# Kernel optimization log

Measured on AMD Instinct MI355X. Metric: run time of the kernel, lower is better.

The kernel has to match this reference:

```python
import jax, jax.numpy as jnp
import numpy as np

V = 50000
K = 24
NB = 10
P = (K - 1) * 9  # 207 pose-blend coefficients
# canonical SMPL kinematic tree (parent[0] is unused / root)
SMPL_PARENT = np.array([0, 0, 0, 0, 1, 2, 3, 4, 5, 6, 7, 8, 9, 9, 9, 12, 13, 14, 16, 17, 18, 19, 20, 21], dtype=np.int64)


def setup_inputs() -> dict:
    key = jax.random.key(0)
    ks = jax.random.split(key, 8)
    betas = jax.random.normal(ks[0], (NB,), dtype=jnp.float32)
    pose = jax.random.normal(ks[1], (K, 3), dtype=jnp.float32) * 0.3
    trans = jax.random.normal(ks[2], (3,), dtype=jnp.float32)
    shapedirs = jax.random.normal(ks[3], (V, 3, NB), dtype=jnp.float32) * 0.01
    v_template = jax.random.normal(ks[4], (V, 3), dtype=jnp.float32)
    J_regressor = jax.random.uniform(ks[5], (K, V), dtype=jnp.float32)
    J_regressor = J_regressor / jnp.sum(J_regressor, axis=1, keepdims=True)
    weights = jax.random.uniform(ks[6], (V, K), dtype=jnp.float32)
    weights = weights / jnp.sum(weights, axis=1, keepdims=True)
    posedirs = jax.random.normal(ks[7], (V, 3, P), dtype=jnp.float32) * 0.01
    return {"betas": betas, "pose": pose, "trans": trans, "shapedirs": shapedirs,
            "v_template": v_template, "J_regressor": J_regressor, "weights": weights,
            "posedirs": posedirs, "parent": SMPL_PARENT}


def rodrigues(r):
    """Axis-angle [K,3] -> rotation matrices [K,3,3]."""
    theta = jnp.linalg.norm(r + 1e-8, axis=-1, keepdims=True)  # [K,1]
    r_hat = r / theta
    x, y, z = r_hat[:, 0], r_hat[:, 1], r_hat[:, 2]
    zero = jnp.zeros_like(x)
    m = jnp.stack([zero, -z, y, z, zero, -x, -y, x, zero], axis=1).reshape(-1, 3, 3)
    cos = jnp.cos(theta)[:, :, None]
    sin = jnp.sin(theta)[:, :, None]
    eye = jnp.eye(3, dtype=r.dtype)[None]
    outer = r_hat[:, :, None] * r_hat[:, None, :]
    return cos * eye + (1.0 - cos) * outer + sin * m


def smpl_forward(betas, pose, trans, shapedirs, v_template, J_regressor, weights, posedirs, parent):
    parent = np.asarray(parent)
    nJ = parent.shape[0]
    v_shaped = jnp.einsum('vki,i->vk', shapedirs, betas) + v_template  # [V,3]
    J = J_regressor @ v_shaped                                          # [K,3]
    R = rodrigues(pose.reshape(-1, 3))                                  # [K,3,3]
    lrotmin = (R[1:] - jnp.eye(3, dtype=R.dtype)[None]).reshape(-1)     # [207]
    v_posed = v_shaped + jnp.einsum('vkp,p->vk', posedirs, lrotmin)

    bottom = jnp.array([[0.0, 0.0, 0.0, 1.0]], dtype=R.dtype)
    def make_A(Ri, t):  # [3,3],[3] -> [4,4]
        return jnp.concatenate([jnp.concatenate([Ri, t[:, None]], axis=1), bottom], axis=0)

    G = [make_A(R[0], J[0])]
    for i in range(1, nJ):  # fixed 24-joint tree, small static loop
        p = int(parent[i])
        G.append(G[p] @ make_A(R[i], J[i] - J[p]))
    stacked = jnp.stack(G, axis=0)                                      # [K,4,4]

    Jh = jnp.concatenate([J, jnp.zeros((nJ, 1), dtype=J.dtype)], axis=1)[:, :, None]  # [K,4,1]
    corr = stacked @ Jh                                                 # [K,4,1]
    pack = jnp.concatenate([jnp.zeros((nJ, 4, 3), dtype=J.dtype), corr], axis=2)
    results = stacked - pack                                            # [K,4,4]

    T = jnp.einsum('vj,jab->vab', weights, results)                     # [V,4,4]
    rest = jnp.concatenate([v_posed, jnp.ones((v_posed.shape[0], 1), dtype=v_posed.dtype)], axis=1)
    v = jnp.einsum('vab,vb->va', T, rest)[:, :3]
    return v + trans[None, :]


def reference(betas, pose, trans, shapedirs, v_template, J_regressor, weights, posedirs, parent):
    return smpl_forward(betas, pose, trans, shapedirs, v_template, J_regressor, weights, posedirs, parent)
```

## Files before the change

### kernel.cpp

```cpp
#include <hip/hip_runtime.h>

#define NV 50000
#define NJ 24
#define NBETA 10
#define NP 207
#define NROWS 150000

#define K1_BLOCKS 196

#define VPB 32
#define RPB 96
#define GPB 24
#define K3_BLOCKS 1563

#define PARTIAL_OFF 0
#define LROT_OFF    14336
#define M_OFF       14592

__device__ const int d_par[NJ] = {0,0,0,0,1,2,3,4,5,6,7,8,9,9,9,12,13,14,16,17,18,19,20,21};
__device__ const int d_lvl[NJ] = {0,1,1,1,2,2,2,3,3,3,4,4,4,4,4,5,5,5,6,6,7,7,8,8};

__global__ __launch_bounds__(256) void k1_partialJ(
    const float* __restrict__ betas, const float* __restrict__ shapedirs,
    const float* __restrict__ v_template, const float* __restrict__ Jreg,
    float* __restrict__ ws)
{
    __shared__ float sd[256 * 30];
    __shared__ float vt[256 * 3];
    __shared__ float bet[NBETA];
    __shared__ float red[4 * 72];

    const int t = threadIdx.x;
    const int blk = blockIdx.x;
    if (t < NBETA) bet[t] = betas[t];

    const int vbase = blk * 256;
    const int nv    = min(256, NV - vbase);
    {
        const int nf4 = (nv * 30) >> 2;
        const float4* sdg = (const float4*)(shapedirs + (size_t)vbase * 30);
        for (int i = t; i < nf4; i += 256) ((float4*)sd)[i] = sdg[i];
        const float* vtg = v_template + (size_t)vbase * 3;
        const int nf3 = nv * 3;
        for (int i = t; i < nf3; i += 256) vt[i] = vtg[i];
    }
    __syncthreads();

    float accJ[72];
#pragma unroll
    for (int q = 0; q < 72; q++) accJ[q] = 0.f;

    const int v = vbase + t;
    if (v < NV) {
        float vs0 = vt[t * 3 + 0], vs1 = vt[t * 3 + 1], vs2 = vt[t * 3 + 2];
#pragma unroll
        for (int i = 0; i < NBETA; i++) {
            const float b = bet[i];
            vs0 += sd[t * 30 + 0 * 10 + i] * b;
            vs1 += sd[t * 30 + 1 * 10 + i] * b;
            vs2 += sd[t * 30 + 2 * 10 + i] * b;
        }
#pragma unroll
        for (int j = 0; j < NJ; j++) {
            const float w = Jreg[(size_t)j * NV + v];
            accJ[j * 3 + 0] += w * vs0;
            accJ[j * 3 + 1] += w * vs1;
            accJ[j * 3 + 2] += w * vs2;
        }
    }

    const int lane = t & 63, wv = t >> 6;
#pragma unroll
    for (int q = 0; q < 72; q++) {
        float x = accJ[q];
#pragma unroll
        for (int m = 1; m < 64; m <<= 1) x += __shfl_xor(x, m);
        if (lane == 0) red[wv * 72 + q] = x;
    }
    __syncthreads();
    if (t < 72)
        ws[PARTIAL_OFF + blk * 72 + t] = red[t] + red[72 + t] + red[144 + t] + red[216 + t];
}

__global__ __launch_bounds__(256) void k2_small(
    const float* __restrict__ pose, float* __restrict__ ws)
{
    __shared__ float Jl[NJ * 3];
    __shared__ float Rl[NJ * 9];
    __shared__ float Gl[NJ * 12];
    const int t = threadIdx.x;

    if (t < 72) {
        float s0 = 0.f, s1 = 0.f;
        for (int b = 0; b < K1_BLOCKS; b += 2) {
            s0 += ws[PARTIAL_OFF + b * 72 + t];
            s1 += ws[PARTIAL_OFF + (b + 1) * 72 + t];
        }
        Jl[t] = s0 + s1;
    }
    __syncthreads();

    if (t < NJ) {
        const float x = pose[t * 3 + 0], y = pose[t * 3 + 1], z = pose[t * 3 + 2];
        const float ex = x + 1e-8f, ey = y + 1e-8f, ez = z + 1e-8f;
        const float theta = sqrtf(ex * ex + ey * ey + ez * ez);
        const float inv = 1.f / theta;
        const float rx = x * inv, ry = y * inv, rz = z * inv;
        const float c = cosf(theta), s = sinf(theta), omc = 1.f - c;
        float R[9];
        R[0] = c + omc * rx * rx;      R[1] = omc * rx * ry - s * rz; R[2] = omc * rx * rz + s * ry;
        R[3] = omc * ry * rx + s * rz; R[4] = c + omc * ry * ry;      R[5] = omc * ry * rz - s * rx;
        R[6] = omc * rz * rx - s * ry; R[7] = omc * rz * ry + s * rx; R[8] = c + omc * rz * rz;
#pragma unroll
        for (int q = 0; q < 9; q++) Rl[t * 9 + q] = R[q];
        if (t >= 1) {
#pragma unroll
            for (int q = 0; q < 9; q++)
                ws[LROT_OFF + (t - 1) * 9 + q] = R[q] - ((q == 0 || q == 4 || q == 8) ? 1.f : 0.f);
        }
    }
    __syncthreads();

    for (int L = 0; L < 9; L++) {
        if (t < NJ && d_lvl[t] == L) {
            if (t == 0) {
#pragma unroll
                for (int r = 0; r < 3; r++) {
                    Gl[r * 4 + 0] = Rl[r * 3 + 0];
                    Gl[r * 4 + 1] = Rl[r * 3 + 1];
                    Gl[r * 4 + 2] = Rl[r * 3 + 2];
                    Gl[r * 4 + 3] = Jl[r];
                }
            } else {
                const int p = d_par[t];
                const float tx = Jl[t * 3 + 0] - Jl[p * 3 + 0];
                const float ty = Jl[t * 3 + 1] - Jl[p * 3 + 1];
                const float tz = Jl[t * 3 + 2] - Jl[p * 3 + 2];
#pragma unroll
                for (int r = 0; r < 3; r++) {
                    const float g0 = Gl[p * 12 + r * 4 + 0];
                    const float g1 = Gl[p * 12 + r * 4 + 1];
                    const float g2 = Gl[p * 12 + r * 4 + 2];
                    const float g3 = Gl[p * 12 + r * 4 + 3];
                    Gl[t * 12 + r * 4 + 0] = g0 * Rl[t * 9 + 0] + g1 * Rl[t * 9 + 3] + g2 * Rl[t * 9 + 6];
                    Gl[t * 12 + r * 4 + 1] = g0 * Rl[t * 9 + 1] + g1 * Rl[t * 9 + 4] + g2 * Rl[t * 9 + 7];
                    Gl[t * 12 + r * 4 + 2] = g0 * Rl[t * 9 + 2] + g1 * Rl[t * 9 + 5] + g2 * Rl[t * 9 + 8];
                    Gl[t * 12 + r * 4 + 3] = g0 * tx + g1 * ty + g2 * tz + g3;
                }
            }
        }
        __syncthreads();
    }

    if (t < NJ) {
        const float jx = Jl[t * 3 + 0], jy = Jl[t * 3 + 1], jz = Jl[t * 3 + 2];
#pragma unroll
        for (int r = 0; r < 3; r++) {
            const float g0 = Gl[t * 12 + r * 4 + 0];
            const float g1 = Gl[t * 12 + r * 4 + 1];
            const float g2 = Gl[t * 12 + r * 4 + 2];
            const float g3 = Gl[t * 12 + r * 4 + 3];
            ws[M_OFF + t * 12 + r * 4 + 0] = g0;
            ws[M_OFF + t * 12 + r * 4 + 1] = g1;
            ws[M_OFF + t * 12 + r * 4 + 2] = g2;
            ws[M_OFF + t * 12 + r * 4 + 3] = g3 - (g0 * jx + g1 * jy + g2 * jz);
        }
    }
}

__global__ __launch_bounds__(256) void k3_fused(
    const float* __restrict__ betas, const float* __restrict__ trans,
    const float* __restrict__ shapedirs, const float* __restrict__ v_template,
    const float* __restrict__ weights, const float* __restrict__ posedirs,
    const float* __restrict__ ws, float* __restrict__ out)
{
    __shared__ float vposed[RPB];
    __shared__ float Ml[288];

    const int t = threadIdx.x;
    const int lane = t & 63, wv = t >> 6;
    const int l16 = lane & 15, g = lane >> 4;
    const int blk = blockIdx.x;

    Ml[t] = ws[M_OFF + t];
    if (t < 32) Ml[256 + t] = ws[M_OFF + 256 + t];

    float lrk[12];
#pragma unroll
    for (int k = 0; k < 12; k++) lrk[k] = ws[LROT_OFF + k * 16 + l16];
    const float lr12 = (l16 < 15) ? ws[LROT_OFF + 192 + l16] : 0.f;
    const float bet  = (l16 < NBETA) ? betas[l16] : 0.f;

    const int gbase = blk * GPB + wv * 6;
#pragma unroll
    for (int i = 0; i < 6; i += 2) {
        const int rowA = (gbase + i) * 4 + g;
        const int rowB = rowA + 4;
        const bool okA = rowA < NROWS;
        const bool okB = rowB < NROWS;

        float va[12], vb[12];
        float tA = 0.f, tB = 0.f, sA = 0.f, sB = 0.f;
        if (okA) {
            const float* pa = posedirs + (size_t)rowA * NP;
#pragma unroll
            for (int k = 0; k < 12; k++) va[k] = pa[k * 16 + l16];
            if (l16 < 15)    tA = pa[192 + l16];
            if (l16 < NBETA) sA = shapedirs[(size_t)rowA * NBETA + l16];
        } else {
#pragma unroll
            for (int k = 0; k < 12; k++) va[k] = 0.f;
        }
        if (okB) {
            const float* pb = posedirs + (size_t)rowB * NP;
#pragma unroll
            for (int k = 0; k < 12; k++) vb[k] = pb[k * 16 + l16];
            if (l16 < 15)    tB = pb[192 + l16];
            if (l16 < NBETA) sB = shapedirs[(size_t)rowB * NBETA + l16];
        } else {
#pragma unroll
            for (int k = 0; k < 12; k++) vb[k] = 0.f;
        }

        float accA = tA * lr12 + sA * bet;
        float accB = tB * lr12 + sB * bet;
#pragma unroll
        for (int k = 0; k < 12; k++) accA += va[k] * lrk[k];
#pragma unroll
        for (int k = 0; k < 12; k++) accB += vb[k] * lrk[k];
#pragma unroll
        for (int m = 1; m < 16; m <<= 1) {
            accA += __shfl_xor(accA, m);
            accB += __shfl_xor(accB, m);
        }
        if (l16 == 0) {
            if (okA) vposed[rowA - blk * RPB] = accA + v_template[rowA];
            if (okB) vposed[rowB - blk * RPB] = accB + v_template[rowB];
        }
    }
    __syncthreads();

    if (t < VPB) {
        const int v = blk * VPB + t;
        if (v < NV) {
            const float4* w4 = (const float4*)(weights + (size_t)v * 24);
            float wj[24];
#pragma unroll
            for (int q = 0; q < 6; q++) {
                const float4 w = w4[q];
                wj[q * 4 + 0] = w.x; wj[q * 4 + 1] = w.y;
                wj[q * 4 + 2] = w.z; wj[q * 4 + 3] = w.w;
            }
            float T[12];
#pragma unroll
            for (int q = 0; q < 12; q++) T[q] = 0.f;
#pragma unroll
            for (int j = 0; j < NJ; j++) {
                const float w = wj[j];
#pragma unroll
                for (int q = 0; q < 12; q++) T[q] += w * Ml[j * 12 + q];
            }
            const float p0 = vposed[t * 3 + 0];
            const float p1 = vposed[t * 3 + 1];
            const float p2 = vposed[t * 3 + 2];
            out[(size_t)v * 3 + 0] = T[0] * p0 + T[1] * p1 + T[2]  * p2 + T[3]  + trans[0];
            out[(size_t)v * 3 + 1] = T[4] * p0 + T[5] * p1 + T[6]  * p2 + T[7]  + trans[1];
            out[(size_t)v * 3 + 2] = T[8] * p0 + T[9] * p1 + T[10] * p2 + T[11] + trans[2];
        }
    }
}

extern "C" void kernel_launch(void* const* d_in, const int* in_sizes, int n_in,
                              void* d_out, int out_size, void* d_ws, size_t ws_size,
                              hipStream_t stream) {
    const float* betas      = (const float*)d_in[0];
    const float* pose       = (const float*)d_in[1];
    const float* trans      = (const float*)d_in[2];
    const float* shapedirs  = (const float*)d_in[3];
    const float* v_template = (const float*)d_in[4];
    const float* Jreg       = (const float*)d_in[5];
    const float* weights    = (const float*)d_in[6];
    const float* posedirs   = (const float*)d_in[7];
    float* ws  = (float*)d_ws;
    float* out = (float*)d_out;

    k1_partialJ<<<dim3(K1_BLOCKS), dim3(256), 0, stream>>>(betas, shapedirs, v_template, Jreg, ws);
    k2_small<<<dim3(1), dim3(256), 0, stream>>>(pose, ws);
    k3_fused<<<dim3(K3_BLOCKS), dim3(256), 0, stream>>>(
        betas, trans, shapedirs, v_template, weights, posedirs, ws, out);
}
```

Before: 55.69 us.

## Load posedirs as float4 per row-group of four rows with whole-wave reduction

The pose-blend GEMV now treats four consecutive posedirs rows (828 floats) as one contiguous block that a whole 64-lane wave reads with float4 loads. The lrot coefficients are replicated four times in the workspace so each lane's float4 lines up with them, and lane-range predicates route each partial product to one of four row accumulators. The goal is fewer, wider, fully coalesced memory transactions on the dominant posedirs stream. In exchange it adds a full 64-lane butterfly reduction over eight accumulators, predicated adds, and moves the v_template add into the skinning stage.

```diff
diff --git a/kernel.cpp b/kernel.cpp
--- a/kernel.cpp
+++ b/kernel.cpp
@@ -5,6 +5,7 @@
 #define NBETA 10
 #define NP 207
 #define NROWS 150000
+#define ROWGROUPS 37500
 
 #define K1_BLOCKS 196
 
@@ -14,8 +15,8 @@
 #define K3_BLOCKS 1563
 
 #define PARTIAL_OFF 0
-#define LROT_OFF    14336
-#define M_OFF       14592
+#define LROT4_OFF   14592
+#define M_OFF       15424
 
 __device__ const int d_par[NJ] = {0,0,0,0,1,2,3,4,5,6,7,8,9,9,9,12,13,14,16,17,18,19,20,21};
 __device__ const int d_lvl[NJ] = {0,1,1,1,2,2,2,3,3,3,4,4,4,4,4,5,5,5,6,6,7,7,8,8};
@@ -88,6 +89,7 @@
     __shared__ float Jl[NJ * 3];
     __shared__ float Rl[NJ * 9];
     __shared__ float Gl[NJ * 12];
+    __shared__ float lrotl[NP];
     const int t = threadIdx.x;
 
     if (t < 72) {
@@ -116,10 +118,18 @@
         if (t >= 1) {
 #pragma unroll
             for (int q = 0; q < 9; q++)
-                ws[LROT_OFF + (t - 1) * 9 + q] = R[q] - ((q == 0 || q == 4 || q == 8) ? 1.f : 0.f);
-        }
-    }
-    __syncthreads();
+                lrotl[(t - 1) * 9 + q] = R[q] - ((q == 0 || q == 4 || q == 8) ? 1.f : 0.f);
+        }
+    }
+    __syncthreads();
+
+    for (int i = t; i < 4 * NP; i += 256) {
+        int c = i;
+        if (c >= 3 * NP) c -= 3 * NP;
+        else if (c >= 2 * NP) c -= 2 * NP;
+        else if (c >= NP) c -= NP;
+        ws[LROT4_OFF + i] = lrotl[c];
+    }
 
     for (int L = 0; L < 9; L++) {
         if (t < NJ && d_lvl[t] == L) {
@@ -179,63 +189,96 @@
 
     const int t = threadIdx.x;
     const int lane = t & 63, wv = t >> 6;
-    const int l16 = lane & 15, g = lane >> 4;
     const int blk = blockIdx.x;
 
     Ml[t] = ws[M_OFF + t];
     if (t < 32) Ml[256 + t] = ws[M_OFF + 256 + t];
 
-    float lrk[12];
-#pragma unroll
-    for (int k = 0; k < 12; k++) lrk[k] = ws[LROT_OFF + k * 16 + l16];
-    const float lr12 = (l16 < 15) ? ws[LROT_OFF + 192 + l16] : 0.f;
-    const float bet  = (l16 < NBETA) ? betas[l16] : 0.f;
+    const float4 z4 = {0.f, 0.f, 0.f, 0.f};
+
+    const float4* E4 = (const float4*)(ws + LROT4_OFF);
+    const float4 e40 = E4[lane];
+    const float4 e41 = E4[64 + lane];
+    const float4 e42 = E4[128 + lane];
+    const float4 e43 = (lane < 15) ? E4[192 + lane] : z4;
+
+    const int bcol = (lane < 10) ? lane : (lane < 20) ? lane - 10 : (lane < 30) ? lane - 20 : lane - 30;
+    const float bscal = (lane < 40) ? betas[bcol] : 0.f;
+
+    auto accum = [&](const float4& q0, const float4& q1, const float4& q2, const float4& q3,
+                     float sv, float& a0, float& a1, float& a2, float& a3) {
+        {
+            const float v0 = q0.x * e40.x, v1 = q0.y * e40.y, v2 = q0.z * e40.z, v3 = q0.w * e40.w;
+            const float s = v0 + v1 + v2;
+            if (lane < 52) a0 += s; else a1 += s;
+            if (lane < 51) a0 += v3; else a1 += v3;
+        }
+        {
+            const float v0 = q1.x * e41.x, v1 = q1.y * e41.y, v2 = q1.z * e41.z, v3 = q1.w * e41.w;
+            const float s01 = v0 + v1, s23 = v2 + v3;
+            if (lane < 40) a1 += s01; else a2 += s01;
+            if (lane < 39) a1 += s23; else a2 += s23;
+        }
+        {
+            const float v0 = q2.x * e42.x, v1 = q2.y * e42.y, v2 = q2.z * e42.z, v3 = q2.w * e42.w;
+            const float s123 = v1 + v2 + v3;
+            if (lane < 28) a2 += v0; else a3 += v0;
+            if (lane < 27) a2 += s123; else a3 += s123;
+        }
+        if (lane < 15) a3 += q3.x * e43.x + q3.y * e43.y + q3.z * e43.z + q3.w * e43.w;
+        {
+            const float v = sv * bscal;
+            if (lane < 10) a0 += v;
+            else if (lane < 20) a1 += v;
+            else if (lane < 30) a2 += v;
+            else if (lane < 40) a3 += v;
+        }
+    };
 
     const int gbase = blk * GPB + wv * 6;
 #pragma unroll
     for (int i = 0; i < 6; i += 2) {
-        const int rowA = (gbase + i) * 4 + g;
-        const int rowB = rowA + 4;
-        const bool okA = rowA < NROWS;
-        const bool okB = rowB < NROWS;
-
-        float va[12], vb[12];
-        float tA = 0.f, tB = 0.f, sA = 0.f, sB = 0.f;
+        const int gA = gbase + i, gB = gA + 1;
+        const bool okA = gA < ROWGROUPS, okB = gB < ROWGROUPS;
+
+        float4 pa0, pa1, pa2, pa3, pb0, pb1, pb2, pb3;
+        float sa = 0.f, sb = 0.f;
         if (okA) {
-            const float* pa = posedirs + (size_t)rowA * NP;
-#pragma unroll
-            for (int k = 0; k < 12; k++) va[k] = pa[k * 16 + l16];
-            if (l16 < 15)    tA = pa[192 + l16];
-            if (l16 < NBETA) sA = shapedirs[(size_t)rowA * NBETA + l16];
-        } else {
-#pragma unroll
-            for (int k = 0; k < 12; k++) va[k] = 0.f;
-        }
+            const float4* G = (const float4*)posedirs + (size_t)gA * 207;
+            pa0 = G[lane]; pa1 = G[64 + lane]; pa2 = G[128 + lane];
+            pa3 = (lane < 15) ? G[192 + lane] : z4;
+            sa  = (lane < 40) ? shapedirs[(size_t)gA * 40 + lane] : 0.f;
+        } else { pa0 = pa1 = pa2 = pa3 = z4; }
         if (okB) {
-            const float* pb = posedirs + (size_t)rowB * NP;
-#pragma unroll
-            for (int k = 0; k < 12; k++) vb[k] = pb[k * 16 + l16];
-            if (l16 < 15)    tB = pb[192 + l16];
-            if (l16 < NBETA) sB = shapedirs[(size_t)rowB * NBETA + l16];
-        } else {
-#pragma unroll
-            for (int k = 0; k < 12; k++) vb[k] = 0.f;
-        }
-
-        float accA = tA * lr12 + sA * bet;
-        float accB = tB * lr12 + sB * bet;
-#pragma unroll
-        for (int k = 0; k < 12; k++) accA += va[k] * lrk[k];
-#pragma unroll
-        for (int k = 0; k < 12; k++) accB += vb[k] * lrk[k];
-#pragma unroll
-        for (int m = 1; m < 16; m <<= 1) {
-            accA += __shfl_xor(accA, m);
-            accB += __shfl_xor(accB, m);
-        }
-        if (l16 == 0) {
-            if (okA) vposed[rowA - blk * RPB] = accA + v_template[rowA];
-            if (okB) vposed[rowB - blk * RPB] = accB + v_template[rowB];
+            const float4* G = (const float4*)posedirs + (size_t)gB * 207;
+            pb0 = G[lane]; pb1 = G[64 + lane]; pb2 = G[128 + lane];
+            pb3 = (lane < 15) ? G[192 + lane] : z4;
+            sb  = (lane < 40) ? shapedirs[(size_t)gB * 40 + lane] : 0.f;
+        } else { pb0 = pb1 = pb2 = pb3 = z4; }
+
+        float a0 = 0.f, a1 = 0.f, a2 = 0.f, a3 = 0.f;
+        float b0 = 0.f, b1 = 0.f, b2 = 0.f, b3 = 0.f;
+        accum(pa0, pa1, pa2, pa3, sa, a0, a1, a2, a3);
+        accum(pb0, pb1, pb2, pb3, sb, b0, b1, b2, b3);
+
+#pragma unroll
+        for (int m = 1; m < 64; m <<= 1) {
+            a0 += __shfl_xor(a0, m); a1 += __shfl_xor(a1, m);
+            a2 += __shfl_xor(a2, m); a3 += __shfl_xor(a3, m);
+            b0 += __shfl_xor(b0, m); b1 += __shfl_xor(b1, m);
+            b2 += __shfl_xor(b2, m); b3 += __shfl_xor(b3, m);
+        }
+        if (lane == 0) {
+            if (okA) {
+                const int gl = gA - blk * GPB;
+                vposed[gl * 4 + 0] = a0; vposed[gl * 4 + 1] = a1;
+                vposed[gl * 4 + 2] = a2; vposed[gl * 4 + 3] = a3;
+            }
+            if (okB) {
+                const int gl = gB - blk * GPB;
+                vposed[gl * 4 + 0] = b0; vposed[gl * 4 + 1] = b1;
+                vposed[gl * 4 + 2] = b2; vposed[gl * 4 + 3] = b3;
+            }
         }
     }
     __syncthreads();
@@ -260,9 +303,9 @@
 #pragma unroll
                 for (int q = 0; q < 12; q++) T[q] += w * Ml[j * 12 + q];
             }
-            const float p0 = vposed[t * 3 + 0];
-            const float p1 = vposed[t * 3 + 1];
-            const float p2 = vposed[t * 3 + 2];
+            const float p0 = vposed[t * 3 + 0] + v_template[(size_t)v * 3 + 0];
+            const float p1 = vposed[t * 3 + 1] + v_template[(size_t)v * 3 + 1];
+            const float p2 = vposed[t * 3 + 2] + v_template[(size_t)v * 3 + 2];
             out[(size_t)v * 3 + 0] = T[0] * p0 + T[1] * p1 + T[2]  * p2 + T[3]  + trans[0];
             out[(size_t)v * 3 + 1] = T[4] * p0 + T[5] * p1 + T[6]  * p2 + T[7]  + trans[1];
             out[(size_t)v * 3 + 2] = T[8] * p0 + T[9] * p1 + T[10] * p2 + T[11] + trans[2];
```

Measured after the change: 80.79 us. +45.1%, slower.
